# Optimization experiments

Hardware: AMD Instinct MI355X
Metric: run time of the kernel (lower is better)

## Reference

```python
import jax, jax.numpy as jnp
import numpy as np

INPUT_DIM = 1024
OUTPUT_DIM = 1024
DEGREE = 8
N_TOKENS = 8192


def setup_inputs() -> dict:
    key = jax.random.key(0)
    k1, k2 = jax.random.split(key)
    x = jax.random.normal(k1, (N_TOKENS, INPUT_DIM), dtype=jnp.float32)
    # xavier_normal_ with gain = 1/(input_dim*(degree+1)) over fan dims (output_dim, degree+1)
    fan_in, fan_out = OUTPUT_DIM, DEGREE + 1  # torch treats dim0/dim1 as fans; scale is tiny anyway
    gain = 1.0 / (INPUT_DIM * (DEGREE + 1))
    std = gain * np.sqrt(2.0 / (INPUT_DIM + OUTPUT_DIM))
    cheby_coeffs = std * jax.random.normal(k2, (INPUT_DIM, OUTPUT_DIM, DEGREE + 1), dtype=jnp.float32)
    return {"x": x, "cheby_coeffs": cheby_coeffs}


def reference(x, cheby_coeffs):
    # x: (..., input_dim) -> y: (..., output_dim)
    degree_p1 = cheby_coeffs.shape[-1]
    theta = jnp.arccos(jnp.tanh(x))                      # (..., i)
    arange = jnp.arange(degree_p1, dtype=x.dtype)        # (d,)
    basis = jnp.cos(theta[..., None] * arange)           # (..., i, d) Chebyshev T_d(tanh(x))
    y = jnp.einsum('...id,iod->...o', basis, cheby_coeffs)
    return y
```

## Files before the change

kernel.cpp:

```cpp
#include <hip/hip_runtime.h>


typedef __bf16 bf16;
typedef __bf16 bf16x8 __attribute__((ext_vector_type(8)));
typedef float f32x2 __attribute__((ext_vector_type(2)));
typedef float f32x4 __attribute__((ext_vector_type(4)));
typedef float f32x16 __attribute__((ext_vector_type(16)));

__device__ __forceinline__ void g2lds16(const void* g, void* l) {
  __builtin_amdgcn_global_load_lds(
      (const __attribute__((address_space(1))) unsigned int*)g,
      (__attribute__((address_space(3))) unsigned int*)l, 16, 0, 0);
}

__device__ __forceinline__ float fast_tanh(float a) {
  float e = __expf(a + a);
  return 1.f - 2.f * __builtin_amdgcn_rcpf(e + 1.f);
}

__global__ __launch_bounds__(256)
void cheby_prep(const float* __restrict__ x, const float* __restrict__ C,
                bf16* __restrict__ Bt, float* __restrict__ bias_p,
                float* __restrict__ th, float* __restrict__ out) {
  const int bid = blockIdx.x, tid = threadIdx.x;
  if (bid >= 1024) {
    const int r = bid - 1024;
    f32x4 v = *(const f32x4*)(x + (size_t)r * 1024 + tid * 4);
    f32x4 t;
    #pragma unroll
    for (int j = 0; j < 4; ++j) t[j] = fast_tanh(v[j]);
    *(f32x2*)(th + (size_t)r * 1024 + tid * 2)       = (f32x2){t.x, t.z};
    *(f32x2*)(th + (size_t)r * 1024 + 512 + tid * 2) = (f32x2){t.y, t.w};
    *(f32x4*)(out + (size_t)r * 1024 + tid * 4) = (f32x4){0.f, 0.f, 0.f, 0.f};
    return;
  }
  __shared__ float tile[32][292];
  const int i0 = (bid >> 5) * 32, o0 = (bid & 31) * 32;
  {
    const int r = tid >> 3, seg = tid & 7;
    const float* src = C + (size_t)(i0 + r) * 9216 + (size_t)o0 * 9 + seg * 36;
    float* dst = &tile[r][seg * 36];
    #pragma unroll
    for (int v = 0; v < 9; ++v) *(f32x4*)(dst + v * 4) = *(const f32x4*)(src + v * 4);
  }
  __syncthreads();
  #pragma unroll
  for (int j = 0; j < 4; ++j) {
    int e = tid + 256 * j;
    int il = e >> 5, ol = e & 31;
    int i = i0 + il, o = o0 + ol;
    bf16x8 v;
    #pragma unroll
    for (int d = 0; d < 8; ++d) v[d] = (bf16)tile[il][ol * 9 + 1 + d];
    size_t idx16 = ((size_t)((o >> 7) * 128 + (i >> 3)) * 8 + (i & 7)) * 128 + (o & 127);
    *(bf16x8*)&Bt[idx16 * 8] = v;
  }
  if (tid < 32) {
    float s = 0.f;
    #pragma unroll
    for (int i = 0; i < 32; ++i) s += tile[i][tid * 9];
    bias_p[(size_t)(bid >> 5) * 1024 + o0 + tid] = s;
  }
}

__global__ __launch_bounds__(256, 4)
void cheby_gemm(const float* __restrict__ th, const bf16* __restrict__ Bt,
                const float* __restrict__ bias_p, float* __restrict__ out) {
  __shared__ bf16 Bs[2][8192];

  const int tid  = threadIdx.x;
  const int lane = tid & 63, w = tid >> 6;
  const int wm = w >> 1, wn = w & 1;
  const int nb = blockIdx.x & 7;
  const int kh = (blockIdx.x >> 3) & 1;
  const int mb = blockIdx.x >> 4;
  const int t0 = mb * 128, o0 = nb * 128;
  const int ml = lane & 31, h = lane >> 5;

  const float* xr0 = th + (size_t)(t0 + wm * 64 + ml) * 1024 + h * 512;
  const float* xr1 = xr0 + 32 * 1024;
  const bf16* btw = Bt + ((size_t)nb * 128 * 1024 + (size_t)w * 256 + lane) * 8;

  const int sbeg = kh * 64, send = sbeg + 64;

  f32x16 acc[2][2];
  #pragma unroll
  for (int a = 0; a < 2; ++a)
    #pragma unroll
    for (int b = 0; b < 2; ++b)
      #pragma unroll
      for (int r = 0; r < 16; ++r) acc[a][b][r] = 0.f;

  f32x4 xv0 = *(const f32x4*)(xr0 + sbeg * 4);
  f32x4 xv1 = *(const f32x4*)(xr1 + sbeg * 4);

  #pragma unroll
  for (int b = 0; b < 4; ++b)
    g2lds16(btw + (size_t)sbeg * 8192 + (size_t)b * 64 * 8,
            &Bs[0][(w * 256 + b * 64) * 8]);

  #pragma unroll 1
  for (int s = sbeg; s < send; ++s) {
    const int bi = (s - sbeg) & 1;
    __syncthreads();
    if (s < send - 1) {
      const bf16* g = btw + (size_t)(s + 1) * 8192;
      #pragma unroll
      for (int b = 0; b < 4; ++b)
        g2lds16(g + (size_t)b * 64 * 8, &Bs[bi ^ 1][(w * 256 + b * 64) * 8]);
    }

    f32x4 sd0 = xv0, sd1 = xv1;
    if (s < send - 1) {
      xv0 = *(const f32x4*)(xr0 + (s + 1) * 4);
      xv1 = *(const f32x4*)(xr1 + (s + 1) * 4);
    }

    bf16x8 afr[2][4];
    #pragma unroll
    for (int ks = 0; ks < 4; ++ks) {
      f32x2 t  = {sd0[ks], sd1[ks]};
      f32x2 t2 = t + t;
      f32x2 prev = {1.f, 1.f}, cur = t;
      #pragma unroll
      for (int j = 0; j < 8; ++j) {
        afr[0][ks][j] = (bf16)cur.x;
        afr[1][ks][j] = (bf16)cur.y;
        f32x2 nx = t2 * cur - prev;
        prev = cur; cur = nx;
      }
    }

    #pragma unroll
    for (int ks = 0; ks < 4; ++ks) {
      const int ce = ((ks * 2 + h) * 128 + wn * 64 + ml) * 8;
      bf16x8 b0 = *(const bf16x8*)&Bs[bi][ce];
      bf16x8 b1 = *(const bf16x8*)&Bs[bi][ce + 32 * 8];
      acc[0][0] = __builtin_amdgcn_mfma_f32_32x32x16_bf16(afr[0][ks], b0, acc[0][0], 0, 0, 0);
      acc[0][1] = __builtin_amdgcn_mfma_f32_32x32x16_bf16(afr[0][ks], b1, acc[0][1], 0, 0, 0);
      acc[1][0] = __builtin_amdgcn_mfma_f32_32x32x16_bf16(afr[1][ks], b0, acc[1][0], 0, 0, 0);
      acc[1][1] = __builtin_amdgcn_mfma_f32_32x32x16_bf16(afr[1][ks], b1, acc[1][1], 0, 0, 0);
    }
  }

  const int c0 = o0 + wn * 64 + ml;
  float bv0 = 0.f, bv1 = 0.f;
  if (kh == 0) {
    #pragma unroll
    for (int p = 0; p < 32; ++p) {
      bv0 += bias_p[(size_t)p * 1024 + c0];
      bv1 += bias_p[(size_t)p * 1024 + c0 + 32];
    }
  }
  #pragma unroll
  for (int mt = 0; mt < 2; ++mt)
    #pragma unroll
    for (int r = 0; r < 16; ++r) {
      int row = t0 + wm * 64 + mt * 32 + (r & 3) + 8 * (r >> 2) + 4 * h;
      float* po = out + (size_t)row * 1024 + c0;
      unsafeAtomicAdd(&po[0],  acc[mt][0][r] + bv0);
      unsafeAtomicAdd(&po[32], acc[mt][1][r] + bv1);
    }
}

__global__ __launch_bounds__(256)
void cheby_naive(const float* __restrict__ x, const float* __restrict__ C,
                 float* __restrict__ out) {
  const int t = blockIdx.x, tid = threadIdx.x;
  float acc[4] = {0.f, 0.f, 0.f, 0.f};
  for (int i = 0; i < 1024; ++i) {
    float th = tanhf(x[(size_t)t * 1024 + i]);
    float T[9]; T[0] = 1.f; T[1] = th;
    #pragma unroll
    for (int d = 2; d < 9; ++d) T[d] = 2.f * th * T[d - 1] - T[d - 2];
    #pragma unroll
    for (int j = 0; j < 4; ++j) {
      const float* cp = &C[((size_t)i * 1024 + tid + j * 256) * 9];
      float s = 0.f;
      #pragma unroll
      for (int d = 0; d < 9; ++d) s += T[d] * cp[d];
      acc[j] += s;
    }
  }
  #pragma unroll
  for (int j = 0; j < 4; ++j) out[(size_t)t * 1024 + tid + j * 256] = acc[j];
}

extern "C" void kernel_launch(void* const* d_in, const int* in_sizes, int n_in,
                              void* d_out, int out_size, void* d_ws, size_t ws_size,
                              hipStream_t stream) {
  (void)in_sizes; (void)n_in; (void)out_size;
  const float* x = (const float*)d_in[0];
  const float* C = (const float*)d_in[1];
  float* out = (float*)d_out;

  const size_t bt_bytes = (size_t)8 * 128 * 1024 * 8 * sizeof(bf16);
  const size_t bp_bytes = (size_t)32 * 1024 * sizeof(float);
  const size_t th_bytes = (size_t)8192 * 1024 * sizeof(float);

  if (ws_size >= bt_bytes + bp_bytes + th_bytes) {
    bf16*  Bt     = (bf16*)d_ws;
    float* bias_p = (float*)((char*)d_ws + bt_bytes);
    float* th     = (float*)((char*)d_ws + bt_bytes + bp_bytes);
    cheby_prep<<<9216, 256, 0, stream>>>(x, C, Bt, bias_p, th, out);
    cheby_gemm<<<1024, 256, 0, stream>>>(th, Bt, bias_p, out);
  } else {
    cheby_naive<<<8192, 256, 0, stream>>>(x, C, out);
  }
}
```

Baseline: 299.3 us.

## Use single-wave GEMM blocks with register-prefetched B and fragment-ordered tanh layout

The GEMM moves from 256-thread blocks with LDS double buffering and a split-K atomic reduction to 64-thread single-wave blocks. Each block computes a 64x64 output tile over the full K range, loads B fragments straight into registers with software double buffering, and writes results with plain stores instead of atomics. The prep kernel now writes tanh values in an MFMA-fragment-ordered layout through an LDS transpose and no longer zeroes the output. The aim is to remove atomic and LDS sync overhead, but each block now reads B from global memory with no sharing across waves, which raises L2 traffic, and blocks are small.

```diff
diff --git a/kernel.cpp b/kernel.cpp
--- a/kernel.cpp
+++ b/kernel.cpp
@@ -7,12 +7,6 @@
 typedef float f32x4 __attribute__((ext_vector_type(4)));
 typedef float f32x16 __attribute__((ext_vector_type(16)));
 
-__device__ __forceinline__ void g2lds16(const void* g, void* l) {
-  __builtin_amdgcn_global_load_lds(
-      (const __attribute__((address_space(1))) unsigned int*)g,
-      (__attribute__((address_space(3))) unsigned int*)l, 16, 0, 0);
-}
-
 __device__ __forceinline__ float fast_tanh(float a) {
   float e = __expf(a + a);
   return 1.f - 2.f * __builtin_amdgcn_rcpf(e + 1.f);
@@ -21,17 +15,41 @@
 __global__ __launch_bounds__(256)
 void cheby_prep(const float* __restrict__ x, const float* __restrict__ C,
                 bf16* __restrict__ Bt, float* __restrict__ bias_p,
-                float* __restrict__ th, float* __restrict__ out) {
+                float* __restrict__ thw) {
   const int bid = blockIdx.x, tid = threadIdx.x;
   if (bid >= 1024) {
-    const int r = bid - 1024;
-    f32x4 v = *(const f32x4*)(x + (size_t)r * 1024 + tid * 4);
-    f32x4 t;
-    #pragma unroll
-    for (int j = 0; j < 4; ++j) t[j] = fast_tanh(v[j]);
-    *(f32x2*)(th + (size_t)r * 1024 + tid * 2)       = (f32x2){t.x, t.z};
-    *(f32x2*)(th + (size_t)r * 1024 + 512 + tid * 2) = (f32x2){t.y, t.w};
-    *(f32x4*)(out + (size_t)r * 1024 + tid * 4) = (f32x4){0.f, 0.f, 0.f, 0.f};
+    const int b2 = bid - 1024;
+    const int mbg = b2 >> 1;
+    const int sh = (b2 & 1) * 64;
+    __shared__ float lt[64][65];
+    for (int c8 = 0; c8 < 8; ++c8) {
+      const int i0 = sh * 8 + c8 * 64;
+      __syncthreads();
+      #pragma unroll
+      for (int p = 0; p < 4; ++p) {
+        int idx = tid + p * 256;
+        int row = idx >> 4, sg = idx & 15;
+        f32x4 v = *(const f32x4*)(x + (size_t)(mbg * 64 + row) * 1024 + i0 + sg * 4);
+        #pragma unroll
+        for (int j = 0; j < 4; ++j) lt[row][sg * 4 + j] = fast_tanh(v[j]);
+      }
+      __syncthreads();
+      #pragma unroll
+      for (int half = 0; half < 2; ++half) {
+        int slot = tid + half * 256;
+        int js = slot >> 6, ln = slot & 63;
+        int ml = ln & 31, h = ln >> 5;
+        f32x4 v0, v1;
+        #pragma unroll
+        for (int ks = 0; ks < 4; ++ks) {
+          v0[ks] = lt[ml][js * 8 + 2 * ks + h];
+          v1[ks] = lt[32 + ml][js * 8 + 2 * ks + h];
+        }
+        size_t off = ((size_t)(mbg * 128 + sh + c8 * 8 + js) * 64 + ln) * 8;
+        *(f32x4*)(thw + off)     = v0;
+        *(f32x4*)(thw + off + 4) = v1;
+      }
+    }
     return;
   }
   __shared__ float tile[32][292];
@@ -63,25 +81,18 @@
   }
 }
 
-__global__ __launch_bounds__(256, 4)
-void cheby_gemm(const float* __restrict__ th, const bf16* __restrict__ Bt,
+__global__ __launch_bounds__(64, 2)
+void cheby_gemm(const float* __restrict__ thw, const bf16* __restrict__ Bt,
                 const float* __restrict__ bias_p, float* __restrict__ out) {
-  __shared__ bf16 Bs[2][8192];
-
-  const int tid  = threadIdx.x;
-  const int lane = tid & 63, w = tid >> 6;
-  const int wm = w >> 1, wn = w & 1;
+  const int lane = threadIdx.x;
+  const int ml = lane & 31, h = lane >> 5;
   const int nb = blockIdx.x & 7;
-  const int kh = (blockIdx.x >> 3) & 1;
+  const int wn = (blockIdx.x >> 3) & 1;
   const int mb = blockIdx.x >> 4;
-  const int t0 = mb * 128, o0 = nb * 128;
-  const int ml = lane & 31, h = lane >> 5;
-
-  const float* xr0 = th + (size_t)(t0 + wm * 64 + ml) * 1024 + h * 512;
-  const float* xr1 = xr0 + 32 * 1024;
-  const bf16* btw = Bt + ((size_t)nb * 128 * 1024 + (size_t)w * 256 + lane) * 8;
-
-  const int sbeg = kh * 64, send = sbeg + 64;
+  const int t0 = mb * 64, o0 = nb * 128 + wn * 64;
+
+  const bf16* btl = Bt + (((size_t)nb * 128 * 8 + h) * 128 + (size_t)wn * 64 + ml) * 8;
+  const float* sp = thw + ((size_t)mb * 128 * 64 + lane) * 8;
 
   f32x16 acc[2][2];
   #pragma unroll
@@ -91,35 +102,33 @@
       #pragma unroll
       for (int r = 0; r < 16; ++r) acc[a][b][r] = 0.f;
 
-  f32x4 xv0 = *(const f32x4*)(xr0 + sbeg * 4);
-  f32x4 xv1 = *(const f32x4*)(xr1 + sbeg * 4);
-
-  #pragma unroll
-  for (int b = 0; b < 4; ++b)
-    g2lds16(btw + (size_t)sbeg * 8192 + (size_t)b * 64 * 8,
-            &Bs[0][(w * 256 + b * 64) * 8]);
-
-  #pragma unroll 1
-  for (int s = sbeg; s < send; ++s) {
-    const int bi = (s - sbeg) & 1;
-    __syncthreads();
-    if (s < send - 1) {
-      const bf16* g = btw + (size_t)(s + 1) * 8192;
-      #pragma unroll
-      for (int b = 0; b < 4; ++b)
-        g2lds16(g + (size_t)b * 64 * 8, &Bs[bi ^ 1][(w * 256 + b * 64) * 8]);
-    }
-
-    f32x4 sd0 = xv0, sd1 = xv1;
-    if (s < send - 1) {
-      xv0 = *(const f32x4*)(xr0 + (s + 1) * 4);
-      xv1 = *(const f32x4*)(xr1 + (s + 1) * 4);
-    }
-
+  bf16x8 bA[4][2], bB[4][2];
+  f32x4 s0a, s0b, s1a, s1b;
+
+  #pragma unroll
+  for (int ks = 0; ks < 4; ++ks)
+    #pragma unroll
+    for (int nt = 0; nt < 2; ++nt)
+      bA[ks][nt] = *(const bf16x8*)(btl + ks * 2048 + nt * 256);
+  s0a = *(const f32x4*)(sp);
+  s0b = *(const f32x4*)(sp + 4);
+
+  auto halfstage = [&](int sload, bf16x8 (&bld)[4][2], f32x4& sla, f32x4& slb,
+                       bf16x8 (&bcur)[4][2], f32x4 sca, f32x4 scb, bool doload) {
+    if (doload) {
+      const bf16* g = btl + (size_t)sload * 8192;
+      #pragma unroll
+      for (int ks = 0; ks < 4; ++ks)
+        #pragma unroll
+        for (int nt = 0; nt < 2; ++nt)
+          bld[ks][nt] = *(const bf16x8*)(g + ks * 2048 + nt * 256);
+      sla = *(const f32x4*)(sp + (size_t)sload * 512);
+      slb = *(const f32x4*)(sp + (size_t)sload * 512 + 4);
+    }
     bf16x8 afr[2][4];
     #pragma unroll
     for (int ks = 0; ks < 4; ++ks) {
-      f32x2 t  = {sd0[ks], sd1[ks]};
+      f32x2 t  = {sca[ks], scb[ks]};
       f32x2 t2 = t + t;
       f32x2 prev = {1.f, 1.f}, cur = t;
       #pragma unroll
@@ -130,36 +139,35 @@
         prev = cur; cur = nx;
       }
     }
-
     #pragma unroll
     for (int ks = 0; ks < 4; ++ks) {
-      const int ce = ((ks * 2 + h) * 128 + wn * 64 + ml) * 8;
-      bf16x8 b0 = *(const bf16x8*)&Bs[bi][ce];
-      bf16x8 b1 = *(const bf16x8*)&Bs[bi][ce + 32 * 8];
-      acc[0][0] = __builtin_amdgcn_mfma_f32_32x32x16_bf16(afr[0][ks], b0, acc[0][0], 0, 0, 0);
-      acc[0][1] = __builtin_amdgcn_mfma_f32_32x32x16_bf16(afr[0][ks], b1, acc[0][1], 0, 0, 0);
-      acc[1][0] = __builtin_amdgcn_mfma_f32_32x32x16_bf16(afr[1][ks], b0, acc[1][0], 0, 0, 0);
-      acc[1][1] = __builtin_amdgcn_mfma_f32_32x32x16_bf16(afr[1][ks], b1, acc[1][1], 0, 0, 0);
-    }
-  }
-
-  const int c0 = o0 + wn * 64 + ml;
+      acc[0][0] = __builtin_amdgcn_mfma_f32_32x32x16_bf16(afr[0][ks], bcur[ks][0], acc[0][0], 0, 0, 0);
+      acc[0][1] = __builtin_amdgcn_mfma_f32_32x32x16_bf16(afr[0][ks], bcur[ks][1], acc[0][1], 0, 0, 0);
+      acc[1][0] = __builtin_amdgcn_mfma_f32_32x32x16_bf16(afr[1][ks], bcur[ks][0], acc[1][0], 0, 0, 0);
+      acc[1][1] = __builtin_amdgcn_mfma_f32_32x32x16_bf16(afr[1][ks], bcur[ks][1], acc[1][1], 0, 0, 0);
+    }
+  };
+
+  #pragma unroll 1
+  for (int s = 0; s < 128; s += 2) {
+    halfstage(s + 1, bB, s1a, s1b, bA, s0a, s0b, true);
+    halfstage(s + 2, bA, s0a, s0b, bB, s1a, s1b, s < 126);
+  }
+
   float bv0 = 0.f, bv1 = 0.f;
-  if (kh == 0) {
-    #pragma unroll
-    for (int p = 0; p < 32; ++p) {
-      bv0 += bias_p[(size_t)p * 1024 + c0];
-      bv1 += bias_p[(size_t)p * 1024 + c0 + 32];
-    }
+  #pragma unroll
+  for (int p = 0; p < 32; ++p) {
+    bv0 += bias_p[(size_t)p * 1024 + o0 + ml];
+    bv1 += bias_p[(size_t)p * 1024 + o0 + 32 + ml];
   }
   #pragma unroll
   for (int mt = 0; mt < 2; ++mt)
     #pragma unroll
     for (int r = 0; r < 16; ++r) {
-      int row = t0 + wm * 64 + mt * 32 + (r & 3) + 8 * (r >> 2) + 4 * h;
-      float* po = out + (size_t)row * 1024 + c0;
-      unsafeAtomicAdd(&po[0],  acc[mt][0][r] + bv0);
-      unsafeAtomicAdd(&po[32], acc[mt][1][r] + bv1);
+      int row = t0 + mt * 32 + (r & 3) + 8 * (r >> 2) + 4 * h;
+      float* po = out + (size_t)row * 1024 + o0 + ml;
+      po[0]  = acc[mt][0][r] + bv0;
+      po[32] = acc[mt][1][r] + bv1;
     }
 }
 
@@ -201,9 +209,9 @@
   if (ws_size >= bt_bytes + bp_bytes + th_bytes) {
     bf16*  Bt     = (bf16*)d_ws;
     float* bias_p = (float*)((char*)d_ws + bt_bytes);
-    float* th     = (float*)((char*)d_ws + bt_bytes + bp_bytes);
-    cheby_prep<<<9216, 256, 0, stream>>>(x, C, Bt, bias_p, th, out);
-    cheby_gemm<<<1024, 256, 0, stream>>>(th, Bt, bias_p, out);
+    float* thw    = (float*)((char*)d_ws + bt_bytes + bp_bytes);
+    cheby_prep<<<1280, 256, 0, stream>>>(x, C, Bt, bias_p, thw);
+    cheby_gemm<<<2048, 64, 0, stream>>>(thw, Bt, bias_p, out);
   } else {
     cheby_naive<<<8192, 256, 0, stream>>>(x, C, out);
   }
```

Result: no change. 294.1 us (-1.7%).
